# Optimization experiments

Measured on AMD Instinct MI355X. Metric: run time of the kernel, lower is better.

The kernel has to match this reference:

```python
import jax, jax.numpy as jnp
import numpy as np

S, B, D, H, DFF = 1024, 8, 1024, 16, 4096
DH = D // H
EPS = 1e-5


def setup_inputs() -> dict:
    key = jax.random.key(0)
    ks = jax.random.split(key, 20)
    w = lambda k, shape: (jax.random.normal(k, shape, jnp.float32) * 0.02)
    return {
        "x": jax.random.normal(ks[0], (S, B, D), jnp.float32),
        "key_padding_mask": jax.random.randint(ks[1], (B, S), 0, 5) == 0,
        "attn_bias": jax.random.uniform(ks[2], (B, 1, S), jnp.float32),
        "Wq": w(ks[3], (D, D)), "bq": jnp.zeros((D,), jnp.float32),
        "Wk": w(ks[4], (D, D)), "bk": jnp.zeros((D,), jnp.float32),
        "Wv": w(ks[5], (D, D)), "bv": jnp.zeros((D,), jnp.float32),
        "Wo": w(ks[6], (D, D)), "bo": jnp.zeros((D,), jnp.float32),
        "W1": w(ks[7], (D, DFF)), "b1": jnp.zeros((DFF,), jnp.float32),
        "W2": w(ks[8], (DFF, D)), "b2": jnp.zeros((D,), jnp.float32),
        "g1": jnp.ones((D,), jnp.float32), "be1": jnp.zeros((D,), jnp.float32),
        "g2": jnp.ones((D,), jnp.float32), "be2": jnp.zeros((D,), jnp.float32),
        "alpha": jnp.asarray(0.1, jnp.float32),
    }


def _ln(x, g, b):
    m = jnp.mean(x, axis=-1, keepdims=True)
    v = jnp.mean(jnp.square(x - m), axis=-1, keepdims=True)
    return (x - m) * jax.lax.rsqrt(v + EPS) * g + b


def reference(x, key_padding_mask, attn_bias, Wq, bq, Wk, bk, Wv, bv, Wo, bo,
              W1, b1, W2, b2, g1, be1, g2, be2, alpha):
    # x: (S, B, D) seq-first; pre-norm attention block
    x2 = _ln(x, g1, be1).transpose(1, 0, 2)  # (B, S, D)
    def heads(W, bias):
        return (x2 @ W + bias).reshape(B, S, H, DH).transpose(0, 2, 1, 3)  # (B,H,S,DH)
    Q, K, V = heads(Wq, bq), heads(Wk, bk), heads(Wv, bv)
    scores = jnp.einsum('bhqd,bhkd->bhqk', Q, K) * (DH ** -0.5)  # (B,H,S,S)
    # attn_bias (B,1,S) -> (B,1,1,S): additive key-side TF-IDF bias
    scores = scores + attn_bias[:, :, None, :] * alpha
    scores = jnp.where(key_padding_mask[:, None, None, :], -jnp.inf, scores)
    attn = jax.nn.softmax(scores, axis=-1)
    out = jnp.einsum('bhqk,bhkd->bhqd', attn, V)  # (B,H,S,DH)
    out = out.transpose(0, 2, 1, 3).reshape(B, S, D)
    out = (out @ Wo + bo).transpose(1, 0, 2)  # back to (S,B,D)
    x = x + out
    # pre-norm FFN block
    h = _ln(x, g2, be2)
    h = jax.nn.relu(h @ W1 + b1) @ W2 + b2
    return x + h
```

## Files before the change

### kernel.cpp

```cpp
#include <hip/hip_runtime.h>
#include <stdint.h>

#define S_LEN 1024
#define BATCH 8
#define DMODEL 1024
#define NHEAD 16
#define DHEAD 64
#define DFF_N 4096
#define EPS 1e-5f

typedef __attribute__((ext_vector_type(8))) short bf16x8;
typedef __attribute__((ext_vector_type(4))) float f32x4;

__device__ __forceinline__ unsigned short f2bf(float f) {
  union { float f; unsigned u; } x; x.f = f;
  unsigned r = x.u + 0x7FFFu + ((x.u >> 16) & 1u);
  return (unsigned short)(r >> 16);
}

__device__ __forceinline__ void gld_lds16(const void* g, void* l) {
  __builtin_amdgcn_global_load_lds(
      (const __attribute__((address_space(1))) void*)g,
      (__attribute__((address_space(3))) void*)l, 16, 0, 0);
}

__global__ __launch_bounds__(256) void transpose_cvt(
    const float* __restrict__ src, unsigned short* __restrict__ dst, int K, int N) {
  __shared__ float tile[32][33];
  int n0 = blockIdx.x * 32, k0 = blockIdx.y * 32;
  int tx = threadIdx.x & 31, ty = threadIdx.x >> 5;
#pragma unroll
  for (int p = 0; p < 4; ++p)
    tile[ty + p * 8][tx] = src[(long)(k0 + ty + p * 8) * N + n0 + tx];
  __syncthreads();
#pragma unroll
  for (int p = 0; p < 4; ++p)
    dst[(long)(n0 + ty + p * 8) * K + k0 + tx] = f2bf(tile[tx][ty + p * 8]);
}

__global__ __launch_bounds__(256) void biasm_kernel(
    const float* __restrict__ bias, const int* __restrict__ kpm,
    const float* __restrict__ alpha_p, float* __restrict__ biasm) {
  int i = blockIdx.x * 256 + threadIdx.x;
  float a = alpha_p[0];
  biasm[i] = kpm[i] ? -1e30f : bias[i] * a;
}

__global__ __launch_bounds__(256) void ln_kernel(
    const float* __restrict__ in, const float* __restrict__ g,
    const float* __restrict__ be, unsigned short* __restrict__ out, int permute) {
  int rr = blockIdx.x;
  long in_off;
  if (permute) { int b = rr >> 10, s = rr & 1023; in_off = ((long)s * BATCH + b) * DMODEL; }
  else in_off = (long)rr * DMODEL;
  int t = threadIdx.x;
  float4 v = *(const float4*)(in + in_off + t * 4);
  float sum = v.x + v.y + v.z + v.w;
#pragma unroll
  for (int m = 1; m < 64; m <<= 1) sum += __shfl_xor(sum, m);
  __shared__ float red[4];
  __shared__ float red2[4];
  int wave = t >> 6, lane = t & 63;
  if (lane == 0) red[wave] = sum;
  __syncthreads();
  sum = red[0] + red[1] + red[2] + red[3];
  float mean = sum * (1.0f / DMODEL);
  float dx = v.x - mean, dy = v.y - mean, dz = v.z - mean, dw = v.w - mean;
  float vs = dx * dx + dy * dy + dz * dz + dw * dw;
#pragma unroll
  for (int m = 1; m < 64; m <<= 1) vs += __shfl_xor(vs, m);
  if (lane == 0) red2[wave] = vs;
  __syncthreads();
  vs = red2[0] + red2[1] + red2[2] + red2[3];
  float rstd = rsqrtf(vs * (1.0f / DMODEL) + EPS);
  float4 gv = *(const float4*)(g + t * 4);
  float4 bv = *(const float4*)(be + t * 4);
  ushort4 pk;
  pk.x = f2bf(dx * rstd * gv.x + bv.x);
  pk.y = f2bf(dy * rstd * gv.y + bv.y);
  pk.z = f2bf(dz * rstd * gv.z + bv.z);
  pk.w = f2bf(dw * rstd * gv.w + bv.w);
  *(ushort4*)(out + (long)rr * DMODEL + t * 4) = pk;
}

#define BM 128
#define BN 128
#define BK 64
#define MODE_QKV 0
#define MODE_OPROJ 1
#define MODE_FFN1 2
#define MODE_FFN2 3

template <int MODE>
__global__ __launch_bounds__(256) void gemm_bt(
    const unsigned short* __restrict__ A, const unsigned short* __restrict__ Bt,
    int M, int N, int K,
    const float* __restrict__ bias0, const float* __restrict__ bias1,
    const float* __restrict__ bias2,
    unsigned short* out_q, unsigned short* out_k, unsigned short* out_vt,
    const float* __restrict__ resid, float* out_f32, unsigned short* out_bf16) {
  __shared__ unsigned short As[BM * BK];
  __shared__ unsigned short Bs[BN * BK];
  int nbx = gridDim.x;
  int nwg = nbx * gridDim.y;
  int orig = blockIdx.y * nbx + blockIdx.x;
  int cpx = nwg >> 3;
  int swz = (orig & 7) * cpx + (orig >> 3);
  int bx = swz % nbx, by = swz / nbx;
  int m0 = by * BM, n0 = bx * BN;
  int t = threadIdx.x, wave = t >> 6, lane = t & 63;
  int wr = wave >> 1, wc = wave & 1;
  const unsigned short* Ab = A + (long)m0 * K;
  const unsigned short* Bb = Bt + (long)n0 * K;
  f32x4 acc[4][4];
#pragma unroll
  for (int i = 0; i < 4; ++i)
#pragma unroll
    for (int j = 0; j < 4; ++j) acc[i][j] = (f32x4){0.f, 0.f, 0.f, 0.f};

  int lrow = lane >> 3;
  int lcol = (lane & 7) * 8;

  auto stage = [&](int kt) {
    long kofs = (long)kt * BK;
#pragma unroll
    for (int j = 0; j < 4; ++j) {
      int rowbase = (j * 4 + wave) * 8;
      gld_lds16(Ab + (long)(rowbase + lrow) * K + kofs + lcol, &As[rowbase * BK]);
      gld_lds16(Bb + (long)(rowbase + lrow) * K + kofs + lcol, &Bs[rowbase * BK]);
    }
  };

  int kt_count = K / BK;
  stage(0);
  for (int kt = 0; kt < kt_count; ++kt) {
    __syncthreads();
#pragma unroll
    for (int kk = 0; kk < 2; ++kk) {
      int ko = kk * 32 + 8 * (lane >> 4);
      bf16x8 a[4], b[4];
#pragma unroll
      for (int i = 0; i < 4; ++i)
        a[i] = *(const bf16x8*)&As[(wr * 64 + i * 16 + (lane & 15)) * BK + ko];
#pragma unroll
      for (int j = 0; j < 4; ++j)
        b[j] = *(const bf16x8*)&Bs[(wc * 64 + j * 16 + (lane & 15)) * BK + ko];
#pragma unroll
      for (int i = 0; i < 4; ++i)
#pragma unroll
        for (int j = 0; j < 4; ++j)
          acc[i][j] = __builtin_amdgcn_mfma_f32_16x16x32_bf16(a[i], b[j], acc[i][j], 0, 0, 0);
    }
    __syncthreads();
    if (kt + 1 < kt_count) stage(kt + 1);
  }

  int rbase = (lane >> 4) << 2;
#pragma unroll
  for (int i = 0; i < 4; ++i) {
#pragma unroll
    for (int j = 0; j < 4; ++j) {
      int mrow = m0 + wr * 64 + i * 16 + rbase;
      int ncol = n0 + wc * 64 + j * 16 + (lane & 15);
      if constexpr (MODE == MODE_QKV) {
        int sel = ncol >> 10, nn = ncol & 1023;
        int h = nn >> 6, dh = nn & 63;
        const float* bptr = (sel == 0) ? bias0 : ((sel == 1) ? bias1 : bias2);
        float bias = bptr[nn];
        if (sel < 2) {
          unsigned short* dst = (sel == 0) ? out_q : out_k;
#pragma unroll
          for (int r = 0; r < 4; ++r) {
            int m = mrow + r; int bb = m >> 10, s = m & 1023;
            dst[(((long)(bb * NHEAD + h)) * S_LEN + s) * DHEAD + dh] = f2bf(acc[i][j][r] + bias);
          }
        } else {
          int m = mrow; int bb = m >> 10, s = m & 1023;
          ushort4 pk;
          pk.x = f2bf(acc[i][j][0] + bias);
          pk.y = f2bf(acc[i][j][1] + bias);
          pk.z = f2bf(acc[i][j][2] + bias);
          pk.w = f2bf(acc[i][j][3] + bias);
          *(ushort4*)&out_vt[(((long)(bb * NHEAD + h)) * DHEAD + dh) * S_LEN + s] = pk;
        }
      } else if constexpr (MODE == MODE_OPROJ) {
        float bias = bias0[ncol];
#pragma unroll
        for (int r = 0; r < 4; ++r) {
          int m = mrow + r; int bb = m >> 10, s = m & 1023;
          long oi = ((long)s * BATCH + bb) * DMODEL + ncol;
          out_f32[oi] = resid[oi] + acc[i][j][r] + bias;
        }
      } else if constexpr (MODE == MODE_FFN1) {
        float bias = bias0[ncol];
#pragma unroll
        for (int r = 0; r < 4; ++r) {
          long m = mrow + r;
          float v = acc[i][j][r] + bias;
          out_bf16[m * (long)N + ncol] = f2bf(v > 0.f ? v : 0.f);
        }
      } else {
        float bias = bias0[ncol];
#pragma unroll
        for (int r = 0; r < 4; ++r) {
          long m = mrow + r;
          long oi = m * (long)N + ncol;
          out_f32[oi] = resid[oi] + acc[i][j][r] + bias;
        }
      }
    }
  }
}

__global__ __launch_bounds__(512, 4) void attn_kernel(
    const unsigned short* __restrict__ qbuf, const unsigned short* __restrict__ kbuf,
    const unsigned short* __restrict__ vtbuf, const float* __restrict__ biasm,
    unsigned short* __restrict__ out) {
  int wave = threadIdx.x >> 6, lane = threadIdx.x & 63;
  int h = blockIdx.y, b = blockIdx.z;
  int q0 = blockIdx.x * 256 + wave * 32;
  long bh = (long)(b * NHEAD + h);
  const unsigned short* Q = qbuf + bh * S_LEN * DHEAD;
  const unsigned short* Kp = kbuf + bh * S_LEN * DHEAD;
  const unsigned short* Vt = vtbuf + bh * DHEAD * S_LEN;
  const float* bm = biasm + (long)b * S_LEN;

  __shared__ unsigned short Ktile[2][64 * 64];
  __shared__ unsigned short Vtile[2][64 * 64];
  __shared__ uint2 Pbuf[8][256];
  __shared__ float AL[8][2][16];
  __shared__ float LI[8][2][16];
  uint2* Pw = Pbuf[wave];

  int qr = lane & 15, g = lane >> 4;

  int srow = wave * 8 + (lane >> 3);
  int scol = (lane & 7) ^ (srow & 7);
  const unsigned short* Ksrc = Kp + (long)srow * DHEAD + scol * 8;
  const unsigned short* Vsrc = Vt + (long)srow * S_LEN + scol * 8;

  bf16x8 qf[2][2];
#pragma unroll
  for (int f = 0; f < 2; ++f)
#pragma unroll
    for (int dhh = 0; dhh < 2; ++dhh)
      qf[f][dhh] = *(const bf16x8*)&Q[(long)(q0 + f * 16 + qr) * DHEAD + dhh * 32 + g * 8];

  f32x4 oacc[2][4];
#pragma unroll
  for (int f = 0; f < 2; ++f)
#pragma unroll
    for (int dt = 0; dt < 4; ++dt) oacc[f][dt] = (f32x4){0.f, 0.f, 0.f, 0.f};
  float m_[2] = {-1e30f, -1e30f}, l_[2] = {0.f, 0.f};

  auto stage = [&](int k0s, int buf) {
    gld_lds16(Ksrc + (long)k0s * DHEAD, (char*)&Ktile[buf][0] + wave * 1024);
    gld_lds16(Vsrc + k0s, (char*)&Vtile[buf][0] + wave * 1024);
  };

  stage(0, 0);
  int cur = 0;
  const int NT = S_LEN / 64;
  for (int t = 0; t < NT; ++t) {
    __syncthreads();
    if (t + 1 < NT) stage((t + 1) * 64, cur ^ 1);

    const char* Kt_l = (const char*)&Ktile[cur][0];
    f32x4 sacc[2][4];
#pragma unroll
    for (int f = 0; f < 2; ++f)
#pragma unroll
      for (int n = 0; n < 4; ++n) sacc[f][n] = (f32x4){0.f, 0.f, 0.f, 0.f};
#pragma unroll
    for (int n = 0; n < 4; ++n)
#pragma unroll
      for (int dhh = 0; dhh < 2; ++dhh) {
        bf16x8 kf = *(const bf16x8*)(Kt_l + (n * 16 + qr) * 128 + (((dhh * 4 + g) ^ (qr & 7)) * 16));
        sacc[0][n] = __builtin_amdgcn_mfma_f32_16x16x32_bf16(kf, qf[0][dhh], sacc[0][n], 0, 0, 0);
        sacc[1][n] = __builtin_amdgcn_mfma_f32_16x16x32_bf16(kf, qf[1][dhh], sacc[1][n], 0, 0, 0);
      }
    float4 bv[4];
#pragma unroll
    for (int n = 0; n < 4; ++n) bv[n] = *(const float4*)&bm[t * 64 + n * 16 + g * 4];

    bf16x8 paf[2][2];
#pragma unroll
    for (int f = 0; f < 2; ++f) {
      float s[16];
#pragma unroll
      for (int n = 0; n < 4; ++n) {
        const float* bvp = (const float*)&bv[n];
#pragma unroll
        for (int r = 0; r < 4; ++r) s[n * 4 + r] = fmaf(sacc[f][n][r], 0.125f, bvp[r]);
      }
      float mx = s[0];
#pragma unroll
      for (int i = 1; i < 16; ++i) mx = fmaxf(mx, s[i]);
      mx = fmaxf(mx, __shfl_xor(mx, 16));
      mx = fmaxf(mx, __shfl_xor(mx, 32));
      float mnew = fmaxf(m_[f], mx);
      float al = __expf(m_[f] - mnew);
      m_[f] = mnew;
      float ps = 0.f;
#pragma unroll
      for (int i = 0; i < 16; ++i) { s[i] = __expf(s[i] - mnew); ps += s[i]; }
      ps += __shfl_xor(ps, 16);
      ps += __shfl_xor(ps, 32);
      l_[f] = l_[f] * al + ps;
      if (lane < 16) AL[wave][f][lane] = al;
#pragma unroll
      for (int n = 0; n < 4; ++n) {
        unsigned w0, w1;
        asm("v_cvt_pk_bf16_f32 %0, %1, %2" : "=v"(w0) : "v"(s[n * 4 + 0]), "v"(s[n * 4 + 1]));
        asm("v_cvt_pk_bf16_f32 %0, %1, %2" : "=v"(w1) : "v"(s[n * 4 + 2]), "v"(s[n * 4 + 3]));
        Pw[qr * 16 + ((n * 4 + g) ^ qr)] = (uint2){w0, w1};
      }
#pragma unroll
      for (int kb = 0; kb < 2; ++kb) {
        union { uint2 u[2]; bf16x8 v; } p;
        p.u[0] = Pw[qr * 16 + ((kb * 8 + g * 2 + 0) ^ qr)];
        p.u[1] = Pw[qr * 16 + ((kb * 8 + g * 2 + 1) ^ qr)];
        paf[f][kb] = p.v;
      }
    }
#pragma unroll
    for (int f = 0; f < 2; ++f) {
      float4 alv = *(const float4*)&AL[wave][f][g * 4];
      const float* ap = (const float*)&alv;
#pragma unroll
      for (int dt = 0; dt < 4; ++dt)
#pragma unroll
        for (int r = 0; r < 4; ++r) oacc[f][dt][r] *= ap[r];
    }
    const char* Vt_l = (const char*)&Vtile[cur][0];
#pragma unroll
    for (int dt = 0; dt < 4; ++dt)
#pragma unroll
      for (int kb = 0; kb < 2; ++kb) {
        bf16x8 vf = *(const bf16x8*)(Vt_l + (dt * 16 + qr) * 128 + (((kb * 4 + g) ^ (qr & 7)) * 16));
        oacc[0][dt] = __builtin_amdgcn_mfma_f32_16x16x32_bf16(paf[0][kb], vf, oacc[0][dt], 0, 0, 0);
        oacc[1][dt] = __builtin_amdgcn_mfma_f32_16x16x32_bf16(paf[1][kb], vf, oacc[1][dt], 0, 0, 0);
      }
    cur ^= 1;
  }

#pragma unroll
  for (int f = 0; f < 2; ++f)
    if (lane < 16) LI[wave][f][lane] = 1.0f / l_[f];
#pragma unroll
  for (int f = 0; f < 2; ++f) {
    float4 lv = *(const float4*)&LI[wave][f][g * 4];
    const float* lp = (const float*)&lv;
#pragma unroll
    for (int dt = 0; dt < 4; ++dt)
#pragma unroll
      for (int r = 0; r < 4; ++r) {
        int q = q0 + f * 16 + g * 4 + r;
        int dh = dt * 16 + qr;
        out[((long)(b * S_LEN + q)) * DMODEL + h * DHEAD + dh] = f2bf(oacc[f][dt][r] * lp[r]);
      }
  }
}

extern "C" void kernel_launch(void* const* d_in, const int* in_sizes, int n_in,
                              void* d_out, int out_size, void* d_ws, size_t ws_size,
                              hipStream_t stream) {
  const float* x  = (const float*)d_in[0];
  const int* kpm  = (const int*)d_in[1];
  const float* attn_bias = (const float*)d_in[2];
  const float* Wq = (const float*)d_in[3];  const float* bq = (const float*)d_in[4];
  const float* Wk = (const float*)d_in[5];  const float* bk = (const float*)d_in[6];
  const float* Wv = (const float*)d_in[7];  const float* bv = (const float*)d_in[8];
  const float* Wo = (const float*)d_in[9];  const float* bo = (const float*)d_in[10];
  const float* W1 = (const float*)d_in[11]; const float* b1 = (const float*)d_in[12];
  const float* W2 = (const float*)d_in[13]; const float* b2 = (const float*)d_in[14];
  const float* g1 = (const float*)d_in[15]; const float* be1 = (const float*)d_in[16];
  const float* g2 = (const float*)d_in[17]; const float* be2 = (const float*)d_in[18];
  const float* alpha = (const float*)d_in[19];
  float* out = (float*)d_out;

  char* ws = (char*)d_ws;
  size_t off = 0;
  auto alloc = [&](size_t bytes) { void* p = ws + off; off += (bytes + 255) & ~(size_t)255; return p; };
  unsigned short* WqkvT = (unsigned short*)alloc(3072ull * 1024 * 2);
  unsigned short* WoT   = (unsigned short*)alloc(1024ull * 1024 * 2);
  unsigned short* W1T   = (unsigned short*)alloc(4096ull * 1024 * 2);
  unsigned short* W2T   = (unsigned short*)alloc(1024ull * 4096 * 2);
  float* biasm          = (float*)alloc(8192ull * 4);
  float* y1             = (float*)alloc(8192ull * 1024 * 4);
  char* region = (char*)alloc(5ull * 16 * 1024 * 1024);
  unsigned short* x2     = (unsigned short*)(region);
  unsigned short* qb     = (unsigned short*)(region + 16ull * 1024 * 1024);
  unsigned short* kb     = (unsigned short*)(region + 32ull * 1024 * 1024);
  unsigned short* vtb    = (unsigned short*)(region + 48ull * 1024 * 1024);
  unsigned short* attn_o = (unsigned short*)(region + 64ull * 1024 * 1024);
  unsigned short* h2     = (unsigned short*)(region);
  unsigned short* ffn1   = (unsigned short*)(region + 16ull * 1024 * 1024);

  transpose_cvt<<<dim3(32, 32), 256, 0, stream>>>(Wq, WqkvT, 1024, 1024);
  transpose_cvt<<<dim3(32, 32), 256, 0, stream>>>(Wk, WqkvT + 1024ull * 1024, 1024, 1024);
  transpose_cvt<<<dim3(32, 32), 256, 0, stream>>>(Wv, WqkvT + 2048ull * 1024, 1024, 1024);
  transpose_cvt<<<dim3(32, 32), 256, 0, stream>>>(Wo, WoT, 1024, 1024);
  transpose_cvt<<<dim3(128, 32), 256, 0, stream>>>(W1, W1T, 1024, 4096);
  transpose_cvt<<<dim3(32, 128), 256, 0, stream>>>(W2, W2T, 4096, 1024);

  biasm_kernel<<<32, 256, 0, stream>>>(attn_bias, kpm, alpha, biasm);
  ln_kernel<<<8192, 256, 0, stream>>>(x, g1, be1, x2, 1);

  gemm_bt<MODE_QKV><<<dim3(3072 / BN, 8192 / BM), 256, 0, stream>>>(
      x2, WqkvT, 8192, 3072, 1024, bq, bk, bv, qb, kb, vtb, nullptr, nullptr, nullptr);

  attn_kernel<<<dim3(S_LEN / 256, NHEAD, BATCH), 512, 0, stream>>>(
      qb, kb, vtb, biasm, attn_o);

  gemm_bt<MODE_OPROJ><<<dim3(1024 / BN, 8192 / BM), 256, 0, stream>>>(
      attn_o, WoT, 8192, 1024, 1024, bo, nullptr, nullptr,
      nullptr, nullptr, nullptr, x, y1, nullptr);

  ln_kernel<<<8192, 256, 0, stream>>>(y1, g2, be2, h2, 0);

  gemm_bt<MODE_FFN1><<<dim3(4096 / BN, 8192 / BM), 256, 0, stream>>>(
      h2, W1T, 8192, 4096, 1024, b1, nullptr, nullptr,
      nullptr, nullptr, nullptr, nullptr, nullptr, ffn1);

  gemm_bt<MODE_FFN2><<<dim3(1024 / BN, 8192 / BM), 256, 0, stream>>>(
      ffn1, W2T, 8192, 1024, 4096, b2, nullptr, nullptr,
      nullptr, nullptr, nullptr, y1, out, nullptr);
}
```

Before: 568.0 us.

## Rewrite GEMM as 8-wave 256x128 kernel with triple-buffered swizzled LDS pipeline

Replaces the 4-wave 128x128 GEMM with an 8-wave kernel using 256x128 output tiles and a three-deep LDS ring buffer. Global-to-LDS loads for tile k+2 are interleaved with the MFMA phases, and explicit barriers plus setprio keep the math waves fed. LDS rows are XOR-swizzled to avoid bank conflicts. The aim is to hide memory latency and raise MFMA utilisation. In exchange it uses more LDS, brings a larger tile quantisation for the N=1024 GEMMs (256 workgroups), and relies on hand-tuned vmcnt counts.

```diff
diff --git a/kernel.cpp b/kernel.cpp
--- a/kernel.cpp
+++ b/kernel.cpp
@@ -83,85 +83,145 @@
   *(ushort4*)(out + (long)rr * DMODEL + t * 4) = pk;
 }
 
-#define BM 128
-#define BN 128
-#define BK 64
 #define MODE_QKV 0
 #define MODE_OPROJ 1
 #define MODE_FFN1 2
 #define MODE_FFN2 3
 
 template <int MODE>
-__global__ __launch_bounds__(256) void gemm_bt(
+__global__ __launch_bounds__(512, 2) void gemm8(
     const unsigned short* __restrict__ A, const unsigned short* __restrict__ Bt,
     int M, int N, int K,
     const float* __restrict__ bias0, const float* __restrict__ bias1,
     const float* __restrict__ bias2,
     unsigned short* out_q, unsigned short* out_k, unsigned short* out_vt,
     const float* __restrict__ resid, float* out_f32, unsigned short* out_bf16) {
-  __shared__ unsigned short As[BM * BK];
-  __shared__ unsigned short Bs[BN * BK];
+  __shared__ unsigned short AS[3][256 * 64];
+  __shared__ unsigned short BS[3][128 * 64];
   int nbx = gridDim.x;
   int nwg = nbx * gridDim.y;
   int orig = blockIdx.y * nbx + blockIdx.x;
   int cpx = nwg >> 3;
   int swz = (orig & 7) * cpx + (orig >> 3);
   int bx = swz % nbx, by = swz / nbx;
-  int m0 = by * BM, n0 = bx * BN;
+  int m0 = by * 256, n0 = bx * 128;
   int t = threadIdx.x, wave = t >> 6, lane = t & 63;
-  int wr = wave >> 1, wc = wave & 1;
+  int wr = wave >> 2, wc = wave & 3;
+  int qr = lane & 15, g = lane >> 4;
   const unsigned short* Ab = A + (long)m0 * K;
   const unsigned short* Bb = Bt + (long)n0 * K;
-  f32x4 acc[4][4];
-#pragma unroll
-  for (int i = 0; i < 4; ++i)
-#pragma unroll
-    for (int j = 0; j < 4; ++j) acc[i][j] = (f32x4){0.f, 0.f, 0.f, 0.f};
-
-  int lrow = lane >> 3;
-  int lcol = (lane & 7) * 8;
-
-  auto stage = [&](int kt) {
-    long kofs = (long)kt * BK;
-#pragma unroll
-    for (int j = 0; j < 4; ++j) {
-      int rowbase = (j * 4 + wave) * 8;
-      gld_lds16(Ab + (long)(rowbase + lrow) * K + kofs + lcol, &As[rowbase * BK]);
-      gld_lds16(Bb + (long)(rowbase + lrow) * K + kofs + lcol, &Bs[rowbase * BK]);
+  int srow = wave * 8 + (lane >> 3);
+  int sgo = ((lane & 7) ^ (lane >> 3)) * 8;
+
+  f32x4 acc[8][2];
+#pragma unroll
+  for (int i = 0; i < 8; ++i)
+#pragma unroll
+    for (int j = 0; j < 2; ++j) acc[i][j] = (f32x4){0.f, 0.f, 0.f, 0.f};
+
+  auto stageA = [&](int kt, int buf, int L) {
+    gld_lds16(Ab + (long)(L * 64 + srow) * K + kt * 64 + sgo,
+              (char*)&AS[buf][0] + L * 8192 + wave * 1024);
+  };
+  auto stageB = [&](int kt, int buf, int L) {
+    gld_lds16(Bb + (long)(L * 64 + srow) * K + kt * 64 + sgo,
+              (char*)&BS[buf][0] + L * 8192 + wave * 1024);
+  };
+  int xh = qr & 7;
+  auto ldA = [&](const char* base, int h, int ii, int ks) {
+    int ra = wr * 128 + (h * 4 + ii) * 16 + qr;
+    return *(const bf16x8*)(base + ra * 128 + ((ks * 4 + g) ^ xh) * 16);
+  };
+  auto ldB = [&](const char* base, int jn, int ks) {
+    int rb = wc * 32 + jn * 16 + qr;
+    return *(const bf16x8*)(base + rb * 128 + ((ks * 4 + g) ^ xh) * 16);
+  };
+
+  const int NT = K / 64;
+#pragma unroll
+  for (int L = 0; L < 4; ++L) stageA(0, 0, L);
+#pragma unroll
+  for (int L = 0; L < 2; ++L) stageB(0, 0, L);
+#pragma unroll
+  for (int L = 0; L < 4; ++L) stageA(1, 1, L);
+#pragma unroll
+  for (int L = 0; L < 2; ++L) stageB(1, 1, L);
+  asm volatile("s_waitcnt vmcnt(6)" ::: "memory");
+  __builtin_amdgcn_sched_barrier(0);
+  __builtin_amdgcn_s_barrier();
+
+  int bread = 0, bstage = 2;
+  for (int kt = 0; kt < NT; ++kt) {
+    const char* Ac = (const char*)&AS[bread][0];
+    const char* Bc = (const char*)&BS[bread][0];
+    bool pf = (kt + 2 < NT);
+    bf16x8 af[4][2], bf0[2], bf1[2];
+#pragma unroll
+    for (int ii = 0; ii < 4; ++ii)
+#pragma unroll
+      for (int ks = 0; ks < 2; ++ks) af[ii][ks] = ldA(Ac, 0, ii, ks);
+#pragma unroll
+    for (int ks = 0; ks < 2; ++ks) bf0[ks] = ldB(Bc, 0, ks);
+    if (pf) { stageA(kt + 2, bstage, 0); stageA(kt + 2, bstage, 1); }
+    __builtin_amdgcn_s_barrier();
+    __builtin_amdgcn_s_setprio(1);
+#pragma unroll
+    for (int ii = 0; ii < 4; ++ii)
+#pragma unroll
+      for (int ks = 0; ks < 2; ++ks)
+        acc[ii][0] = __builtin_amdgcn_mfma_f32_16x16x32_bf16(af[ii][ks], bf0[ks], acc[ii][0], 0, 0, 0);
+    __builtin_amdgcn_s_setprio(0);
+    __builtin_amdgcn_s_barrier();
+#pragma unroll
+    for (int ks = 0; ks < 2; ++ks) bf1[ks] = ldB(Bc, 1, ks);
+    if (pf) { stageA(kt + 2, bstage, 2); stageA(kt + 2, bstage, 3); }
+    __builtin_amdgcn_s_barrier();
+    __builtin_amdgcn_s_setprio(1);
+#pragma unroll
+    for (int ii = 0; ii < 4; ++ii)
+#pragma unroll
+      for (int ks = 0; ks < 2; ++ks)
+        acc[ii][1] = __builtin_amdgcn_mfma_f32_16x16x32_bf16(af[ii][ks], bf1[ks], acc[ii][1], 0, 0, 0);
+    __builtin_amdgcn_s_setprio(0);
+    __builtin_amdgcn_s_barrier();
+#pragma unroll
+    for (int ii = 0; ii < 4; ++ii)
+#pragma unroll
+      for (int ks = 0; ks < 2; ++ks) af[ii][ks] = ldA(Ac, 1, ii, ks);
+    if (pf) { stageB(kt + 2, bstage, 0); stageB(kt + 2, bstage, 1); }
+    __builtin_amdgcn_s_barrier();
+    __builtin_amdgcn_s_setprio(1);
+#pragma unroll
+    for (int ii = 0; ii < 4; ++ii)
+#pragma unroll
+      for (int ks = 0; ks < 2; ++ks)
+        acc[4 + ii][1] = __builtin_amdgcn_mfma_f32_16x16x32_bf16(af[ii][ks], bf1[ks], acc[4 + ii][1], 0, 0, 0);
+    __builtin_amdgcn_s_setprio(0);
+    __builtin_amdgcn_s_barrier();
+    __builtin_amdgcn_s_setprio(1);
+#pragma unroll
+    for (int ii = 0; ii < 4; ++ii)
+#pragma unroll
+      for (int ks = 0; ks < 2; ++ks)
+        acc[4 + ii][0] = __builtin_amdgcn_mfma_f32_16x16x32_bf16(af[ii][ks], bf0[ks], acc[4 + ii][0], 0, 0, 0);
+    __builtin_amdgcn_s_setprio(0);
+    if (kt + 2 < NT) {
+      asm volatile("s_waitcnt vmcnt(6)" ::: "memory");
+    } else if (kt + 2 == NT) {
+      asm volatile("s_waitcnt vmcnt(0)" ::: "memory");
     }
-  };
-
-  int kt_count = K / BK;
-  stage(0);
-  for (int kt = 0; kt < kt_count; ++kt) {
-    __syncthreads();
-#pragma unroll
-    for (int kk = 0; kk < 2; ++kk) {
-      int ko = kk * 32 + 8 * (lane >> 4);
-      bf16x8 a[4], b[4];
-#pragma unroll
-      for (int i = 0; i < 4; ++i)
-        a[i] = *(const bf16x8*)&As[(wr * 64 + i * 16 + (lane & 15)) * BK + ko];
-#pragma unroll
-      for (int j = 0; j < 4; ++j)
-        b[j] = *(const bf16x8*)&Bs[(wc * 64 + j * 16 + (lane & 15)) * BK + ko];
-#pragma unroll
-      for (int i = 0; i < 4; ++i)
-#pragma unroll
-        for (int j = 0; j < 4; ++j)
-          acc[i][j] = __builtin_amdgcn_mfma_f32_16x16x32_bf16(a[i], b[j], acc[i][j], 0, 0, 0);
-    }
-    __syncthreads();
-    if (kt + 1 < kt_count) stage(kt + 1);
+    __builtin_amdgcn_sched_barrier(0);
+    __builtin_amdgcn_s_barrier();
+    bread = (bread == 2) ? 0 : bread + 1;
+    bstage = (bstage == 2) ? 0 : bstage + 1;
   }
 
-  int rbase = (lane >> 4) << 2;
-#pragma unroll
-  for (int i = 0; i < 4; ++i) {
-#pragma unroll
-    for (int j = 0; j < 4; ++j) {
-      int mrow = m0 + wr * 64 + i * 16 + rbase;
-      int ncol = n0 + wc * 64 + j * 16 + (lane & 15);
+#pragma unroll
+  for (int i = 0; i < 8; ++i) {
+#pragma unroll
+    for (int j = 0; j < 2; ++j) {
+      int mrow = m0 + wr * 128 + i * 16 + g * 4;
+      int ncol = n0 + wc * 32 + j * 16 + qr;
       if constexpr (MODE == MODE_QKV) {
         int sel = ncol >> 10, nn = ncol & 1023;
         int h = nn >> 6, dh = nn & 63;
@@ -407,23 +467,23 @@
   biasm_kernel<<<32, 256, 0, stream>>>(attn_bias, kpm, alpha, biasm);
   ln_kernel<<<8192, 256, 0, stream>>>(x, g1, be1, x2, 1);
 
-  gemm_bt<MODE_QKV><<<dim3(3072 / BN, 8192 / BM), 256, 0, stream>>>(
+  gemm8<MODE_QKV><<<dim3(3072 / 128, 8192 / 256), 512, 0, stream>>>(
       x2, WqkvT, 8192, 3072, 1024, bq, bk, bv, qb, kb, vtb, nullptr, nullptr, nullptr);
 
   attn_kernel<<<dim3(S_LEN / 256, NHEAD, BATCH), 512, 0, stream>>>(
       qb, kb, vtb, biasm, attn_o);
 
-  gemm_bt<MODE_OPROJ><<<dim3(1024 / BN, 8192 / BM), 256, 0, stream>>>(
+  gemm8<MODE_OPROJ><<<dim3(1024 / 128, 8192 / 256), 512, 0, stream>>>(
       attn_o, WoT, 8192, 1024, 1024, bo, nullptr, nullptr,
       nullptr, nullptr, nullptr, x, y1, nullptr);
 
   ln_kernel<<<8192, 256, 0, stream>>>(y1, g2, be2, h2, 0);
 
-  gemm_bt<MODE_FFN1><<<dim3(4096 / BN, 8192 / BM), 256, 0, stream>>>(
+  gemm8<MODE_FFN1><<<dim3(4096 / 128, 8192 / 256), 512, 0, stream>>>(
       h2, W1T, 8192, 4096, 1024, b1, nullptr, nullptr,
       nullptr, nullptr, nullptr, nullptr, nullptr, ffn1);
 
-  gemm_bt<MODE_FFN2><<<dim3(1024 / BN, 8192 / BM), 256, 0, stream>>>(
+  gemm8<MODE_FFN2><<<dim3(1024 / 128, 8192 / 256), 512, 0, stream>>>(
       ffn1, W2T, 8192, 1024, 4096, b2, nullptr, nullptr,
       nullptr, nullptr, nullptr, y1, out, nullptr);
 }
```

New measurement: 560.8 us. No clear change (-1.3%).

## Replace GEMM with 8-wave ping-pong pipelined kernel using larger tiles and LDS swizzle

Applied to the files above, without the earlier changes.

Replaces the 128x128 single-buffered GEMM with a 512-thread kernel using 256x128 (or 256x256 for FFN1) tiles. Global-to-LDS loads are double-buffered and prefetched two k-steps ahead. Loads are interleaved with MFMA quadrants separated by barriers, and s_setprio raises priority during MFMA work. An XOR swizzle on LDS columns avoids bank conflicts. The aim is to hide memory latency and increase data reuse, at the cost of more registers and LDS per block and tricky manual waitcnt accounting.

```diff
diff --git a/kernel.cpp b/kernel.cpp
--- a/kernel.cpp
+++ b/kernel.cpp
@@ -23,6 +23,8 @@
       (const __attribute__((address_space(1))) void*)g,
       (__attribute__((address_space(3))) void*)l, 16, 0, 0);
 }
+
+#define BARRIER asm volatile("s_barrier" ::: "memory")
 
 __global__ __launch_bounds__(256) void transpose_cvt(
     const float* __restrict__ src, unsigned short* __restrict__ dst, int K, int N) {
@@ -83,85 +85,173 @@
   *(ushort4*)(out + (long)rr * DMODEL + t * 4) = pk;
 }
 
-#define BM 128
-#define BN 128
-#define BK 64
 #define MODE_QKV 0
 #define MODE_OPROJ 1
 #define MODE_FFN1 2
 #define MODE_FFN2 3
 
-template <int MODE>
-__global__ __launch_bounds__(256) void gemm_bt(
+#define QUADW(MH, NH) do { \
+  _Pragma("unroll") for (int i_ = 0; i_ < 4; ++i_) \
+  _Pragma("unroll") for (int j_ = 0; j_ < 2; ++j_) \
+  _Pragma("unroll") for (int k_ = 0; k_ < 2; ++k_) \
+    acc[(MH) * 4 + i_][(NH) * 2 + j_] = __builtin_amdgcn_mfma_f32_16x16x32_bf16( \
+        af[i_][k_], bfr[NH][j_][k_], acc[(MH) * 4 + i_][(NH) * 2 + j_], 0, 0, 0); \
+} while (0)
+
+#define QUADN(MH) do { \
+  _Pragma("unroll") for (int i_ = 0; i_ < 2; ++i_) \
+  _Pragma("unroll") for (int n_ = 0; n_ < 2; ++n_) \
+  _Pragma("unroll") for (int j_ = 0; j_ < 2; ++j_) \
+  _Pragma("unroll") for (int k_ = 0; k_ < 2; ++k_) \
+    acc[(MH) * 2 + i_][n_ * 2 + j_] = __builtin_amdgcn_mfma_f32_16x16x32_bf16( \
+        af[i_][k_], bfr[n_][j_][k_], acc[(MH) * 2 + i_][n_ * 2 + j_], 0, 0, 0); \
+} while (0)
+
+template <int MODE, bool WIDE>
+__global__ __launch_bounds__(512, 2) void gemm_ph(
     const unsigned short* __restrict__ A, const unsigned short* __restrict__ Bt,
-    int M, int N, int K,
+    int N, int K,
     const float* __restrict__ bias0, const float* __restrict__ bias1,
     const float* __restrict__ bias2,
     unsigned short* out_q, unsigned short* out_k, unsigned short* out_vt,
     const float* __restrict__ resid, float* out_f32, unsigned short* out_bf16) {
-  __shared__ unsigned short As[BM * BK];
-  __shared__ unsigned short Bs[BN * BK];
+  constexpr int BNv = WIDE ? 256 : 128;
+  constexpr int NM = WIDE ? 4 : 2;
+  constexpr int BSLOT = WIDE ? 16384 : 8192;
+  __shared__ unsigned short AS[32768];
+  __shared__ unsigned short BS[WIDE ? 32768 : 16384];
+  char* ASb = (char*)AS;
+  char* BSb = (char*)BS;
+
   int nbx = gridDim.x;
   int nwg = nbx * gridDim.y;
   int orig = blockIdx.y * nbx + blockIdx.x;
-  int cpx = nwg >> 3;
-  int swz = (orig & 7) * cpx + (orig >> 3);
+  int swz = (orig & 7) * (nwg >> 3) + (orig >> 3);
   int bx = swz % nbx, by = swz / nbx;
-  int m0 = by * BM, n0 = bx * BN;
-  int t = threadIdx.x, wave = t >> 6, lane = t & 63;
-  int wr = wave >> 1, wc = wave & 1;
-  const unsigned short* Ab = A + (long)m0 * K;
-  const unsigned short* Bb = Bt + (long)n0 * K;
-  f32x4 acc[4][4];
-#pragma unroll
-  for (int i = 0; i < 4; ++i)
+  int m0 = by * 256, n0 = bx * BNv;
+  int tid = threadIdx.x, wave = tid >> 6, lane = tid & 63;
+  int qr = lane & 15, g = lane >> 4, xh = qr & 7;
+  int wr = WIDE ? (wave >> 2) : (wave >> 1);
+  int wc = WIDE ? (wave & 3) : (wave & 1);
+  int srow = wave * 8 + (lane >> 3);
+  int sgo = ((lane & 7) ^ (lane >> 3)) * 8;
+  const long rK64 = (long)K * 64;
+  const unsigned short* AbS = A + (long)m0 * K + (long)srow * K + sgo;
+  const unsigned short* BbS = Bt + (long)n0 * K + (long)srow * K + sgo;
+  int c0 = (g ^ xh) * 16;
+  int c1 = ((4 + g) ^ xh) * 16;
+  int roA = (WIDE ? wr * 64 : wr * 32) + qr;
+  int roB = wc * 32 + qr;
+
+  f32x4 acc[2 * NM][4];
+#pragma unroll
+  for (int i = 0; i < 2 * NM; ++i)
 #pragma unroll
     for (int j = 0; j < 4; ++j) acc[i][j] = (f32x4){0.f, 0.f, 0.f, 0.f};
-
-  int lrow = lane >> 3;
-  int lcol = (lane & 7) * 8;
-
-  auto stage = [&](int kt) {
-    long kofs = (long)kt * BK;
-#pragma unroll
-    for (int j = 0; j < 4; ++j) {
-      int rowbase = (j * 4 + wave) * 8;
-      gld_lds16(Ab + (long)(rowbase + lrow) * K + kofs + lcol, &As[rowbase * BK]);
-      gld_lds16(Bb + (long)(rowbase + lrow) * K + kofs + lcol, &Bs[rowbase * BK]);
+  bf16x8 af[NM][2];
+  bf16x8 bfr[2][2][2];
+
+  auto stA = [&](int kt, int slot, int L) {
+    gld_lds16(AbS + slot * 2 * rK64 + L * rK64 + kt * 64,
+              ASb + ((kt & 1) * 2 + slot) * 16384 + L * 8192 + wave * 1024);
+  };
+  auto stB = [&](int kt, int slot, int L) {
+    if constexpr (WIDE)
+      gld_lds16(BbS + slot * 2 * rK64 + L * rK64 + kt * 64,
+                BSb + ((kt & 1) * 2 + slot) * 16384 + L * 8192 + wave * 1024);
+    else
+      gld_lds16(BbS + slot * rK64 + kt * 64,
+                BSb + ((kt & 1) * 2 + slot) * 8192 + wave * 1024);
+  };
+  auto ldAh = [&](int buf, int mh) {
+    const char* base = ASb + (buf * 2 + mh) * 16384 + roA * 128;
+#pragma unroll
+    for (int i = 0; i < NM; ++i) {
+      af[i][0] = *(const bf16x8*)(base + i * 2048 + c0);
+      af[i][1] = *(const bf16x8*)(base + i * 2048 + c1);
     }
   };
-
-  int kt_count = K / BK;
-  stage(0);
-  for (int kt = 0; kt < kt_count; ++kt) {
-    __syncthreads();
-#pragma unroll
-    for (int kk = 0; kk < 2; ++kk) {
-      int ko = kk * 32 + 8 * (lane >> 4);
-      bf16x8 a[4], b[4];
-#pragma unroll
-      for (int i = 0; i < 4; ++i)
-        a[i] = *(const bf16x8*)&As[(wr * 64 + i * 16 + (lane & 15)) * BK + ko];
-#pragma unroll
-      for (int j = 0; j < 4; ++j)
-        b[j] = *(const bf16x8*)&Bs[(wc * 64 + j * 16 + (lane & 15)) * BK + ko];
-#pragma unroll
-      for (int i = 0; i < 4; ++i)
-#pragma unroll
-        for (int j = 0; j < 4; ++j)
-          acc[i][j] = __builtin_amdgcn_mfma_f32_16x16x32_bf16(a[i], b[j], acc[i][j], 0, 0, 0);
+  auto ldBh = [&](bf16x8 (&bq)[2][2], int buf, int nh) {
+    const char* base = BSb + (buf * 2 + nh) * BSLOT + roB * 128;
+#pragma unroll
+    for (int j = 0; j < 2; ++j) {
+      bq[j][0] = *(const bf16x8*)(base + j * 2048 + c0);
+      bq[j][1] = *(const bf16x8*)(base + j * 2048 + c1);
     }
-    __syncthreads();
-    if (kt + 1 < kt_count) stage(kt + 1);
+  };
+
+  const int NT = K / 64;
+  if constexpr (WIDE) {
+    stA(0, 0, 0); stA(0, 0, 1); stA(0, 1, 0); stA(0, 1, 1);
+    stB(0, 0, 0); stB(0, 0, 1); stB(0, 1, 0); stB(0, 1, 1);
+    stA(1, 0, 0); stA(1, 0, 1); stB(1, 0, 0); stB(1, 0, 1); stB(1, 1, 0); stB(1, 1, 1);
+    asm volatile("s_waitcnt vmcnt(6)" ::: "memory");
+  } else {
+    stA(0, 0, 0); stA(0, 0, 1); stA(0, 1, 0); stA(0, 1, 1);
+    stB(0, 0, 0); stB(0, 1, 0);
+    stA(1, 0, 0); stA(1, 0, 1); stB(1, 0, 0); stB(1, 1, 0);
+    asm volatile("s_waitcnt vmcnt(4)" ::: "memory");
   }
-
-  int rbase = (lane >> 4) << 2;
-#pragma unroll
-  for (int i = 0; i < 4; ++i) {
-#pragma unroll
-    for (int j = 0; j < 4; ++j) {
-      int mrow = m0 + wr * 64 + i * 16 + rbase;
-      int ncol = n0 + wc * 64 + j * 16 + (lane & 15);
+  __builtin_amdgcn_sched_barrier(0);
+  BARRIER;
+
+  for (int kt = 0; kt < NT; ++kt) {
+    int buf = kt & 1;
+    if constexpr (WIDE) {
+      ldAh(buf, 0);
+      ldBh(bfr[0], buf, 0);
+      if (kt + 1 < NT) { stA(kt + 1, 1, 0); stA(kt + 1, 1, 1); }
+      BARRIER; __builtin_amdgcn_sched_barrier(0);
+      __builtin_amdgcn_s_setprio(1); QUADW(0, 0); __builtin_amdgcn_s_setprio(0);
+      BARRIER;
+      ldBh(bfr[1], buf, 1);
+      if (kt + 2 < NT) { stA(kt + 2, 0, 0); stA(kt + 2, 0, 1); }
+      BARRIER; __builtin_amdgcn_sched_barrier(0);
+      __builtin_amdgcn_s_setprio(1); QUADW(0, 1); __builtin_amdgcn_s_setprio(0);
+      BARRIER;
+      ldAh(buf, 1);
+      if (kt + 2 < NT) { stB(kt + 2, 0, 0); stB(kt + 2, 0, 1); }
+      BARRIER; __builtin_amdgcn_sched_barrier(0);
+      __builtin_amdgcn_s_setprio(1); QUADW(1, 1); __builtin_amdgcn_s_setprio(0);
+      BARRIER;
+      if (kt + 2 < NT) { stB(kt + 2, 1, 0); stB(kt + 2, 1, 1); }
+      BARRIER; __builtin_amdgcn_sched_barrier(0);
+      __builtin_amdgcn_s_setprio(1); QUADW(1, 0); __builtin_amdgcn_s_setprio(0);
+      if (kt + 2 < NT) asm volatile("s_waitcnt vmcnt(6)" ::: "memory");
+      else asm volatile("s_waitcnt vmcnt(0)" ::: "memory");
+      __builtin_amdgcn_sched_barrier(0);
+      BARRIER;
+    } else {
+      ldAh(buf, 0);
+      ldBh(bfr[0], buf, 0);
+      ldBh(bfr[1], buf, 1);
+      if (kt + 1 < NT) { stA(kt + 1, 1, 0); stA(kt + 1, 1, 1); }
+      BARRIER; __builtin_amdgcn_sched_barrier(0);
+      __builtin_amdgcn_s_setprio(1); QUADN(0); __builtin_amdgcn_s_setprio(0);
+      BARRIER;
+      ldAh(buf, 1);
+      if (kt + 2 < NT) { stA(kt + 2, 0, 0); stA(kt + 2, 0, 1); stB(kt + 2, 0, 0); stB(kt + 2, 1, 0); }
+      BARRIER; __builtin_amdgcn_sched_barrier(0);
+      __builtin_amdgcn_s_setprio(1); QUADN(1); __builtin_amdgcn_s_setprio(0);
+      if (kt + 2 < NT) asm volatile("s_waitcnt vmcnt(4)" ::: "memory");
+      else asm volatile("s_waitcnt vmcnt(0)" ::: "memory");
+      __builtin_amdgcn_sched_barrier(0);
+      BARRIER;
+    }
+  }
+
+#pragma unroll
+  for (int I = 0; I < 2 * NM; ++I) {
+#pragma unroll
+    for (int J = 0; J < 4; ++J) {
+      int mrow, ncol;
+      if constexpr (WIDE) {
+        mrow = m0 + (I >> 2) * 128 + wr * 64 + (I & 3) * 16 + g * 4;
+        ncol = n0 + (J >> 1) * 128 + wc * 32 + (J & 1) * 16 + qr;
+      } else {
+        mrow = m0 + (I >> 1) * 128 + wr * 32 + (I & 1) * 16 + g * 4;
+        ncol = n0 + (J >> 1) * 64 + wc * 32 + (J & 1) * 16 + qr;
+      }
       if constexpr (MODE == MODE_QKV) {
         int sel = ncol >> 10, nn = ncol & 1023;
         int h = nn >> 6, dh = nn & 63;
@@ -172,15 +262,15 @@
 #pragma unroll
           for (int r = 0; r < 4; ++r) {
             int m = mrow + r; int bb = m >> 10, s = m & 1023;
-            dst[(((long)(bb * NHEAD + h)) * S_LEN + s) * DHEAD + dh] = f2bf(acc[i][j][r] + bias);
+            dst[(((long)(bb * NHEAD + h)) * S_LEN + s) * DHEAD + dh] = f2bf(acc[I][J][r] + bias);
           }
         } else {
           int m = mrow; int bb = m >> 10, s = m & 1023;
           ushort4 pk;
-          pk.x = f2bf(acc[i][j][0] + bias);
-          pk.y = f2bf(acc[i][j][1] + bias);
-          pk.z = f2bf(acc[i][j][2] + bias);
-          pk.w = f2bf(acc[i][j][3] + bias);
+          pk.x = f2bf(acc[I][J][0] + bias);
+          pk.y = f2bf(acc[I][J][1] + bias);
+          pk.z = f2bf(acc[I][J][2] + bias);
+          pk.w = f2bf(acc[I][J][3] + bias);
           *(ushort4*)&out_vt[(((long)(bb * NHEAD + h)) * DHEAD + dh) * S_LEN + s] = pk;
         }
       } else if constexpr (MODE == MODE_OPROJ) {
@@ -189,14 +279,14 @@
         for (int r = 0; r < 4; ++r) {
           int m = mrow + r; int bb = m >> 10, s = m & 1023;
           long oi = ((long)s * BATCH + bb) * DMODEL + ncol;
-          out_f32[oi] = resid[oi] + acc[i][j][r] + bias;
+          out_f32[oi] = resid[oi] + acc[I][J][r] + bias;
         }
       } else if constexpr (MODE == MODE_FFN1) {
         float bias = bias0[ncol];
 #pragma unroll
         for (int r = 0; r < 4; ++r) {
           long m = mrow + r;
-          float v = acc[i][j][r] + bias;
+          float v = acc[I][J][r] + bias;
           out_bf16[m * (long)N + ncol] = f2bf(v > 0.f ? v : 0.f);
         }
       } else {
@@ -205,7 +295,7 @@
         for (int r = 0; r < 4; ++r) {
           long m = mrow + r;
           long oi = m * (long)N + ncol;
-          out_f32[oi] = resid[oi] + acc[i][j][r] + bias;
+          out_f32[oi] = resid[oi] + acc[I][J][r] + bias;
         }
       }
     }
@@ -407,23 +497,23 @@
   biasm_kernel<<<32, 256, 0, stream>>>(attn_bias, kpm, alpha, biasm);
   ln_kernel<<<8192, 256, 0, stream>>>(x, g1, be1, x2, 1);
 
-  gemm_bt<MODE_QKV><<<dim3(3072 / BN, 8192 / BM), 256, 0, stream>>>(
-      x2, WqkvT, 8192, 3072, 1024, bq, bk, bv, qb, kb, vtb, nullptr, nullptr, nullptr);
+  gemm_ph<MODE_QKV, false><<<dim3(3072 / 128, 32), 512, 0, stream>>>(
+      x2, WqkvT, 3072, 1024, bq, bk, bv, qb, kb, vtb, nullptr, nullptr, nullptr);
 
   attn_kernel<<<dim3(S_LEN / 256, NHEAD, BATCH), 512, 0, stream>>>(
       qb, kb, vtb, biasm, attn_o);
 
-  gemm_bt<MODE_OPROJ><<<dim3(1024 / BN, 8192 / BM), 256, 0, stream>>>(
-      attn_o, WoT, 8192, 1024, 1024, bo, nullptr, nullptr,
+  gemm_ph<MODE_OPROJ, false><<<dim3(1024 / 128, 32), 512, 0, stream>>>(
+      attn_o, WoT, 1024, 1024, bo, nullptr, nullptr,
       nullptr, nullptr, nullptr, x, y1, nullptr);
 
   ln_kernel<<<8192, 256, 0, stream>>>(y1, g2, be2, h2, 0);
 
-  gemm_bt<MODE_FFN1><<<dim3(4096 / BN, 8192 / BM), 256, 0, stream>>>(
-      h2, W1T, 8192, 4096, 1024, b1, nullptr, nullptr,
+  gemm_ph<MODE_FFN1, true><<<dim3(4096 / 256, 32), 512, 0, stream>>>(
+      h2, W1T, 4096, 1024, b1, nullptr, nullptr,
       nullptr, nullptr, nullptr, nullptr, nullptr, ffn1);
 
-  gemm_bt<MODE_FFN2><<<dim3(1024 / BN, 8192 / BM), 256, 0, stream>>>(
-      ffn1, W2T, 8192, 1024, 4096, b2, nullptr, nullptr,
+  gemm_ph<MODE_FFN2, false><<<dim3(1024 / 128, 32), 512, 0, stream>>>(
+      ffn1, W2T, 1024, 4096, b2, nullptr, nullptr,
       nullptr, nullptr, nullptr, y1, out, nullptr);
 }
```

After: 499.7 us. 1.14x faster.
